# Optimization experiments

Measured on AMD Instinct MI355X. Metric: run time of the kernel, lower is better.

The kernel has to match this reference:

```python
import jax, jax.numpy as jnp
import numpy as np

N, T = 4096, 128
D, R = 8, 32
ENC_H, NADE_H, K_MIX = 64, 64, 10


def setup_inputs() -> dict:
    key = jax.random.key(0)
    ks = jax.random.split(key, 17)
    s = 0.1
    rn = lambda k, shp, sc: (sc * jax.random.normal(k, shp)).astype(jnp.float32)
    return {
        "x": rn(ks[0], (N, 1, T), 1.0),
        "enc1_w": rn(ks[1], (1, ENC_H), s),
        "enc1_b": rn(ks[2], (ENC_H,), s),
        "enc2_w": rn(ks[3], (ENC_H, D), s),
        "enc2_b": rn(ks[4], (D,), s),
        "A": rn(ks[5], (R, D, R), s),
        "init_w": rn(ks[6], (1, R), s),
        "nade1_w": rn(ks[7], (R, NADE_H), s),
        "nade1_b": rn(ks[8], (NADE_H,), s),
        "nade2_w": rn(ks[9], (NADE_H, NADE_H), s),
        "nade2_b": rn(ks[10], (NADE_H,), s),
        "mu_w": rn(ks[11], (NADE_H, K_MIX), s),
        "mu_b": rn(ks[12], (K_MIX,), s),
        "sig_w": rn(ks[13], (NADE_H, K_MIX), s),
        "sig_b": rn(ks[14], (K_MIX,), s),
        "alpha_w": rn(ks[15], (NADE_H, K_MIX), s),
        "alpha_b": rn(ks[16], (K_MIX,), s),
    }


def reference(x, enc1_w, enc1_b, enc2_w, enc2_b, A, init_w,
              nade1_w, nade1_b, nade2_w, nade2_b,
              mu_w, mu_b, sig_w, sig_b, alpha_w, alpha_b):
    LOG2PI = jnp.log(2.0 * jnp.pi).astype(x.dtype)

    def phi(x_t, h):
        # x_t: [N], h: [N, R] -> mixture-of-Gaussians log prob [N]
        h = jnp.tanh(h)
        h = jax.nn.relu(h @ nade1_w + nade1_b)
        h = jax.nn.relu(h @ nade2_w + nade2_b)
        mu = h @ mu_w + mu_b                       # [N, K]
        log_sig = h @ sig_w + sig_b                # sig = exp(log_sig)
        log_alpha = jax.nn.log_softmax(h @ alpha_w + alpha_b, axis=1)
        z = (x_t[:, None] - mu) * jnp.exp(-log_sig)
        comp_lp = -0.5 * z * z - log_sig - 0.5 * LOG2PI
        return jax.scipy.special.logsumexp(log_alpha + comp_lp, axis=1)

    xt = x[:, 0, :]                                # [N, T]
    # vectorized encoder over all timesteps: tanh(relu(x*W1+b1)@W2+b2) -> [N, T, D]
    e = jax.nn.relu(xt[:, :, None] * enc1_w[0] + enc1_b)
    enc = jnp.tanh(e @ enc2_w + enc2_b)

    h0 = jnp.broadcast_to(init_w, (xt.shape[0], R))
    res0 = phi(xt[:, 0], h0)

    def step(carry, inputs):
        tmp, res = carry
        e_prev, x_cur = inputs                     # [N, D], [N]
        tmp = jnp.einsum('nd,ni,idj->nj', e_prev, tmp, A)
        res = res + phi(x_cur, tmp)
        return (tmp, res), None

    xs = (jnp.moveaxis(enc[:, :-1, :], 1, 0),      # [T-1, N, D]
          jnp.moveaxis(xt[:, 1:], 1, 0))           # [T-1, N]
    (_, res), _ = jax.lax.scan(step, (h0, res0), xs)
    return jnp.exp(res)
```

## Files before the change

kernel.cpp:

```cpp
#include <hip/hip_runtime.h>

#define DEV __device__ __forceinline__

typedef __attribute__((ext_vector_type(8))) short short8v;
typedef __attribute__((ext_vector_type(4))) float f32x4;

DEV unsigned short bfr(float f) {
    unsigned u = __float_as_uint(f);
    return (unsigned short)((u + 0x7fffu + ((u >> 16) & 1u)) >> 16);
}
DEV short bft(float f) { return (short)(__float_as_uint(f) >> 16); }
DEV float bf2f(unsigned short h) { return __uint_as_float(((unsigned)h) << 16); }
DEV float frcp(float x) { return __builtin_amdgcn_rcpf(x); }
DEV float ftanh(float x) { float e = __expf(2.0f * x); return 1.0f - 2.0f * frcp(e + 1.0f); }

constexpr int NN = 4096, TT = 128;
#define MFMA32(a, b, c) __builtin_amdgcn_mfma_f32_16x16x32_bf16(a, b, c, 0, 0, 0)


__global__ __launch_bounds__(512) __attribute__((amdgpu_waves_per_eu(2)))
void wfa_kernel(
    const float* __restrict__ x,
    const float* __restrict__ e1w, const float* __restrict__ e1b,
    const float* __restrict__ e2w, const float* __restrict__ e2b,
    const float* __restrict__ A,
    const float* __restrict__ initw,
    const float* __restrict__ n1w, const float* __restrict__ n1b,
    const float* __restrict__ n2w, const float* __restrict__ n2b,
    const float* __restrict__ muw, const float* __restrict__ mub,
    const float* __restrict__ sgw, const float* __restrict__ sgb,
    const float* __restrict__ alw, const float* __restrict__ alb,
    float* __restrict__ out)
{
    __shared__ __align__(16) unsigned short enc_l[TT * 128];
    __shared__ __align__(16) float x_l[16 * 130];
    __shared__ __align__(16) short8v ring_l[2][8][64];
    __shared__ __align__(16) float n1b_l[64], n2b_l[64], hb_l[48];
    __shared__ float part_l[8][16];

    const int tid = threadIdx.x;
    const int wv = tid >> 6, lane = tid & 63;
    const int quad = lane >> 4, col = lane & 15;
    const int n0 = blockIdx.x * 16;
    const f32x4 z4 = {0.f, 0.f, 0.f, 0.f};

    for (int i = tid; i < 16 * TT; i += 512)
        x_l[(i >> 7) * 130 + (i & 127)] = x[(n0 + (i >> 7)) * TT + (i & 127)];
    if (tid < 64) { n1b_l[tid] = n1b[tid]; n2b_l[tid] = n2b[tid]; }
    if (tid >= 64 && tid < 112) {
        const int i = tid - 64, mt = i >> 4, k = i & 15;
        hb_l[i] = (k < 10) ? ((mt == 0) ? mub[k] : (mt == 1) ? sgb[k] : alb[k]) : 0.f;
    }

    __syncthreads();

    {
        float e1c[16], e1bc[16];
        #pragma unroll
        for (int kc = 0; kc < 2; ++kc)
            #pragma unroll
            for (int jj = 0; jj < 8; ++jj) {
                const int f = kc * 32 + (jj >> 2) * 16 + quad * 4 + (jj & 3);
                e1c[kc * 8 + jj] = e1w[f];
                e1bc[kc * 8 + jj] = e1b[f];
            }
        short8v E2A[2];
        #pragma unroll
        for (int kc = 0; kc < 2; ++kc)
            #pragma unroll
            for (int jj = 0; jj < 8; ++jj)
                E2A[kc][jj] = (short)(col < 8
                    ? bfr(e2w[(kc * 32 + (jj >> 2) * 16 + quad * 4 + (jj & 3)) * 8 + col]) : 0);
        float e2bc[4];
        #pragma unroll
        for (int r = 0; r < 4; ++r) e2bc[r] = (quad < 2) ? e2b[quad * 4 + r] : 0.f;

        const int tbase = wv * 16;
        #pragma unroll 1
        for (int nn = 0; nn < 16; ++nn) {
            const float xs = x_l[nn * 130 + tbase + col];
            short8v eB[2];
            #pragma unroll
            for (int kc = 0; kc < 2; ++kc)
                #pragma unroll
                for (int jj = 0; jj < 8; ++jj)
                    eB[kc][jj] = bft(fmaxf(fmaf(xs, e1c[kc * 8 + jj], e1bc[kc * 8 + jj]), 0.f));
            f32x4 d = MFMA32(E2A[0], eB[0], z4);
            d = MFMA32(E2A[1], eB[1], d);
            if (quad < 2) {
                #pragma unroll
                for (int r = 0; r < 4; ++r)
                    enc_l[(tbase + col) * 128 + nn * 8 + quad * 4 + r] = bfr(ftanh(d[r] + e2bc[r]));
            }
        }
    }
    __syncthreads();

    if (wv == 0) {
        short8v A2f[16];
        #pragma unroll
        for (int mt = 0; mt < 16; ++mt)
            #pragma unroll
            for (int jj = 0; jj < 8; ++jj)
                A2f[mt][jj] = (short)bfr(
                    A[((jj >> 2) * 16 + quad * 4 + (jj & 3)) * 256 + (mt >> 1) * 32 + (mt & 1) * 16 + col]);

        short8v tmpB;
        #pragma unroll
        for (int jj = 0; jj < 8; ++jj)
            tmpB[jj] = (short)bfr(initw[(jj >> 2) * 16 + quad * 4 + (jj & 3)]);

        asm volatile("s_setprio 2");

        short8v e8c = *(const short8v*)&enc_l[0 * 128 + col * 8];

        #pragma unroll 1
        for (int b = 0; b <= 16; ++b) {
            if (b < 16) {
                #pragma unroll 1
                for (int i = 0; i < 8; ++i) {
                    const int t = b * 8 + i;
                    if (t > 0) {
                        const short8v e8n = *(const short8v*)&enc_l[t * 128 + col * 8];
                        float ev[8];
                        #pragma unroll
                        for (int d = 0; d < 8; ++d) ev[d] = bf2f((unsigned short)e8c[d]);
                        short8v nt;
                        #pragma unroll
                        for (int h = 0; h < 2; ++h) {
                            f32x4 D[8];
                            #pragma unroll
                            for (int d = 0; d < 8; ++d) D[d] = MFMA32(A2f[2 * d + h], tmpB, z4);
                            #pragma unroll
                            for (int r = 0; r < 4; ++r) {
                                float s = 0.f;
                                #pragma unroll
                                for (int d = 0; d < 8; ++d) s = fmaf(ev[d], D[d][r], s);
                                nt[h * 4 + r] = bft(s);
                            }
                        }
                        tmpB = nt;
                        e8c = e8n;
                    }
                    ring_l[b & 1][i][lane] = tmpB;
                }
            }
            __syncthreads();
        }
        if (lane < 16) part_l[0][lane] = 0.f;
    } else {
        short8v W1f[4];
        #pragma unroll
        for (int mt = 0; mt < 4; ++mt)
            #pragma unroll
            for (int jj = 0; jj < 8; ++jj)
                W1f[mt][jj] = (short)bfr(n1w[((jj >> 2) * 16 + quad * 4 + (jj & 3)) * 64 + mt * 16 + col]);
        short8v W2f[4][2];
        #pragma unroll
        for (int mt = 0; mt < 4; ++mt)
            #pragma unroll
            for (int kb = 0; kb < 2; ++kb)
                #pragma unroll
                for (int jj = 0; jj < 8; ++jj)
                    W2f[mt][kb][jj] = (short)bfr(
                        n2w[(kb * 32 + (jj >> 2) * 16 + quad * 4 + (jj & 3)) * 64 + mt * 16 + col]);
        short8v Whf[3][2];
        #pragma unroll
        for (int mt = 0; mt < 3; ++mt) {
            const float* Wh = (mt == 0) ? muw : (mt == 1) ? sgw : alw;
            #pragma unroll
            for (int kb = 0; kb < 2; ++kb)
                #pragma unroll
                for (int jj = 0; jj < 8; ++jj)
                    Whf[mt][kb][jj] = (short)(col < 10
                        ? bfr(Wh[(kb * 32 + (jj >> 2) * 16 + quad * 4 + (jj & 3)) * 10 + col]) : 0);
        }

        float res2 = 0.f;
        const float CST = 0.91893853320467274f;

        #pragma unroll 1
        for (int b = 0; b <= 16; ++b) {
            if (b >= 1) {
                #pragma unroll 1
                for (int i = wv - 1; i < 8; i += 7) {
                    const int t = (b - 1) * 8 + i;
                    const short8v tf = ring_l[(b - 1) & 1][i][lane];
                    short8v thB;
                    #pragma unroll
                    for (int jj = 0; jj < 8; ++jj)
                        thB[jj] = bft(ftanh(bf2f((unsigned short)tf[jj])));

                    short8v h1B[2];
                    #pragma unroll
                    for (int mt = 0; mt < 4; ++mt) {
                        const f32x4 c = *(const f32x4*)&n1b_l[mt * 16 + quad * 4];
                        const f32x4 d = MFMA32(W1f[mt], thB, c);
                        #pragma unroll
                        for (int r = 0; r < 4; ++r)
                            h1B[mt >> 1][(mt & 1) * 4 + r] = bft(fmaxf(d[r], 0.f));
                    }
                    short8v h2B[2];
                    #pragma unroll
                    for (int mt = 0; mt < 4; ++mt) {
                        const f32x4 c = *(const f32x4*)&n2b_l[mt * 16 + quad * 4];
                        f32x4 d = MFMA32(W2f[mt][0], h1B[0], c);
                        d = MFMA32(W2f[mt][1], h1B[1], d);
                        #pragma unroll
                        for (int r = 0; r < 4; ++r)
                            h2B[mt >> 1][(mt & 1) * 4 + r] = bft(fmaxf(d[r], 0.f));
                    }
                    f32x4 hd[3];
                    #pragma unroll
                    for (int mt = 0; mt < 3; ++mt) {
                        const f32x4 c = *(const f32x4*)&hb_l[mt * 16 + quad * 4];
                        f32x4 d = MFMA32(Whf[mt][0], h2B[0], c);
                        hd[mt] = MFMA32(Whf[mt][1], h2B[1], d);
                    }
                    const float xt = x_l[col * 130 + t];
                    float s1 = 0.f, s2 = 0.f;
                    #pragma unroll
                    for (int r = 0; r < 4; ++r) {
                        const bool valid = (quad * 4 + r) < 10;
                        const float mu = hd[0][r], sg = hd[1][r], la = hd[2][r];
                        const float e1t = __expf(la);
                        const float z = (xt - mu) * __expf(-sg);
                        const float e2t = __expf(la - sg - fmaf(0.5f * z, z, CST));
                        s1 += valid ? e1t : 0.f;
                        s2 += valid ? e2t : 0.f;
                    }
                    s1 += __shfl_xor(s1, 16, 64);  s2 += __shfl_xor(s2, 16, 64);
                    s1 += __shfl_xor(s1, 32, 64);  s2 += __shfl_xor(s2, 32, 64);
                    res2 += __log2f(s2) - __log2f(s1);
                }
            }
            __syncthreads();
        }
        if (lane < 16) part_l[wv][lane] = res2;
    }

    __syncthreads();
    if (tid < 16) {
        float s = 0.f;
        #pragma unroll
        for (int w = 0; w < 8; ++w) s += part_l[w][tid];
        out[n0 + tid] = exp2f(s);
    }
}

extern "C" void kernel_launch(void* const* d_in, const int* in_sizes, int n_in,
                              void* d_out, int out_size, void* d_ws, size_t ws_size,
                              hipStream_t stream) {
    wfa_kernel<<<dim3(NN / 16), dim3(512), 0, stream>>>(
        (const float*)d_in[0],  (const float*)d_in[1],  (const float*)d_in[2],
        (const float*)d_in[3],  (const float*)d_in[4],  (const float*)d_in[5],
        (const float*)d_in[6],  (const float*)d_in[7],  (const float*)d_in[8],
        (const float*)d_in[9],  (const float*)d_in[10], (const float*)d_in[11],
        (const float*)d_in[12], (const float*)d_in[13], (const float*)d_in[14],
        (const float*)d_in[15], (const float*)d_in[16], (float*)d_out);
}
```

Measured before the change: 141.1 us.

## Replace block barriers with LDS flag handshakes and deepen the producer ring

Removes the per-batch __syncthreads between the recurrence wave and the NADE consumer waves. Each side now signals through shared-memory flags and progress counters, spinning with s_sleep while it waits. The ring buffer grows from 2 to 4 slots, so the serial recurrence wave can run ahead of the consumers, and it can start once only the encoder rows it needs are ready. The recurrence also issues all 16 MFMAs at once and reduces them with a tree of FMAs. Spin-waiting on LDS flags depends on correct fencing and memory ordering, and polling adds LDS traffic.

```diff
diff --git a/kernel.cpp b/kernel.cpp
--- a/kernel.cpp
+++ b/kernel.cpp
@@ -15,8 +15,16 @@
 DEV float ftanh(float x) { float e = __expf(2.0f * x); return 1.0f - 2.0f * frcp(e + 1.0f); }
 
 constexpr int NN = 4096, TT = 128;
+constexpr int BATCH = 8, NB = TT / BATCH;
+constexpr int RING = 4;
+
 #define MFMA32(a, b, c) __builtin_amdgcn_mfma_f32_16x16x32_bf16(a, b, c, 0, 0, 0)
 
+
+DEV void wait_ge(const unsigned* p, unsigned v) {
+    volatile const unsigned* vp = (volatile const unsigned*)p;
+    while (*vp < v) { asm volatile("s_sleep 2"); }
+}
 
 __global__ __launch_bounds__(512) __attribute__((amdgpu_waves_per_eu(2)))
 void wfa_kernel(
@@ -34,9 +42,12 @@
 {
     __shared__ __align__(16) unsigned short enc_l[TT * 128];
     __shared__ __align__(16) float x_l[16 * 130];
-    __shared__ __align__(16) short8v ring_l[2][8][64];
+    __shared__ __align__(16) short8v ring_l[RING][BATCH][64];
     __shared__ __align__(16) float n1b_l[64], n2b_l[64], hb_l[48];
     __shared__ float part_l[8][16];
+    __shared__ unsigned rf_l[NB];
+    __shared__ unsigned encf_l[8];
+    __shared__ unsigned prog_l[8];
 
     const int tid = threadIdx.x;
     const int wv = tid >> 6, lane = tid & 63;
@@ -51,7 +62,9 @@
         const int i = tid - 64, mt = i >> 4, k = i & 15;
         hb_l[i] = (k < 10) ? ((mt == 0) ? mub[k] : (mt == 1) ? sgb[k] : alb[k]) : 0.f;
     }
-
+    if (tid >= 112 && tid < 112 + NB) rf_l[tid - 112] = 0;
+    if (tid >= 112 + NB && tid < 120 + NB) encf_l[tid - 112 - NB] = 0;
+    if (tid >= 120 + NB && tid < 128 + NB) prog_l[tid - 120 - NB] = 0;
     __syncthreads();
 
     {
@@ -93,8 +106,9 @@
                     enc_l[(tbase + col) * 128 + nn * 8 + quad * 4 + r] = bfr(ftanh(d[r] + e2bc[r]));
             }
         }
-    }
-    __syncthreads();
+        __threadfence_block();
+        if (lane == 0) ((volatile unsigned*)encf_l)[wv] = 1;
+    }
 
     if (wv == 0) {
         short8v A2f[16];
@@ -112,40 +126,54 @@
 
         asm volatile("s_setprio 2");
 
-        short8v e8c = *(const short8v*)&enc_l[0 * 128 + col * 8];
+        float evc[8];
+        {
+            const short8v e80 = *(const short8v*)&enc_l[0 * 128 + col * 8];
+            #pragma unroll
+            for (int d = 0; d < 8; ++d) evc[d] = bf2f((unsigned short)e80[d]);
+        }
 
         #pragma unroll 1
-        for (int b = 0; b <= 16; ++b) {
-            if (b < 16) {
-                #pragma unroll 1
-                for (int i = 0; i < 8; ++i) {
-                    const int t = b * 8 + i;
-                    if (t > 0) {
-                        const short8v e8n = *(const short8v*)&enc_l[t * 128 + col * 8];
-                        float ev[8];
+        for (int b = 0; b < NB; ++b) {
+            wait_ge(&encf_l[(8 * b + 6) >> 4], 1);
+            if (b >= RING) {
+                const unsigned need = (unsigned)(b - (RING - 1));
+                for (;;) {
+                    unsigned m = 0xffffffffu;
+                    #pragma unroll
+                    for (int w = 1; w < 8; ++w)
+                        m = min(m, ((volatile unsigned*)prog_l)[w]);
+                    if (m >= need) break;
+                    asm volatile("s_sleep 2");
+                }
+            }
+            #pragma unroll 1
+            for (int i = 0; i < BATCH; ++i) {
+                const int t = b * BATCH + i;
+                if (t > 0) {
+                    const short8v e8n = *(const short8v*)&enc_l[t * 128 + col * 8];
+                    f32x4 D[16];
+                    #pragma unroll
+                    for (int mt = 0; mt < 16; ++mt) D[mt] = MFMA32(A2f[mt], tmpB, z4);
+                    short8v nt;
+                    #pragma unroll
+                    for (int h = 0; h < 2; ++h)
                         #pragma unroll
-                        for (int d = 0; d < 8; ++d) ev[d] = bf2f((unsigned short)e8c[d]);
-                        short8v nt;
-                        #pragma unroll
-                        for (int h = 0; h < 2; ++h) {
-                            f32x4 D[8];
-                            #pragma unroll
-                            for (int d = 0; d < 8; ++d) D[d] = MFMA32(A2f[2 * d + h], tmpB, z4);
-                            #pragma unroll
-                            for (int r = 0; r < 4; ++r) {
-                                float s = 0.f;
-                                #pragma unroll
-                                for (int d = 0; d < 8; ++d) s = fmaf(ev[d], D[d][r], s);
-                                nt[h * 4 + r] = bft(s);
-                            }
+                        for (int r = 0; r < 4; ++r) {
+                            const float p0 = fmaf(evc[1], D[2 + h][r], evc[0] * D[h][r]);
+                            const float p1 = fmaf(evc[3], D[6 + h][r], evc[2] * D[4 + h][r]);
+                            const float p2 = fmaf(evc[5], D[10 + h][r], evc[4] * D[8 + h][r]);
+                            const float p3 = fmaf(evc[7], D[14 + h][r], evc[6] * D[12 + h][r]);
+                            nt[h * 4 + r] = bft((p0 + p1) + (p2 + p3));
                         }
-                        tmpB = nt;
-                        e8c = e8n;
-                    }
-                    ring_l[b & 1][i][lane] = tmpB;
-                }
-            }
-            __syncthreads();
+                    tmpB = nt;
+                    #pragma unroll
+                    for (int d = 0; d < 8; ++d) evc[d] = bf2f((unsigned short)e8n[d]);
+                }
+                ring_l[b & (RING - 1)][i][lane] = tmpB;
+            }
+            __threadfence_block();
+            if (lane == 0) ((volatile unsigned*)rf_l)[b] = 1;
         }
         if (lane < 16) part_l[0][lane] = 0.f;
     } else {
@@ -180,61 +208,60 @@
         const float CST = 0.91893853320467274f;
 
         #pragma unroll 1
-        for (int b = 0; b <= 16; ++b) {
-            if (b >= 1) {
-                #pragma unroll 1
-                for (int i = wv - 1; i < 8; i += 7) {
-                    const int t = (b - 1) * 8 + i;
-                    const short8v tf = ring_l[(b - 1) & 1][i][lane];
-                    short8v thB;
-                    #pragma unroll
-                    for (int jj = 0; jj < 8; ++jj)
-                        thB[jj] = bft(ftanh(bf2f((unsigned short)tf[jj])));
-
-                    short8v h1B[2];
-                    #pragma unroll
-                    for (int mt = 0; mt < 4; ++mt) {
-                        const f32x4 c = *(const f32x4*)&n1b_l[mt * 16 + quad * 4];
-                        const f32x4 d = MFMA32(W1f[mt], thB, c);
-                        #pragma unroll
-                        for (int r = 0; r < 4; ++r)
-                            h1B[mt >> 1][(mt & 1) * 4 + r] = bft(fmaxf(d[r], 0.f));
-                    }
-                    short8v h2B[2];
-                    #pragma unroll
-                    for (int mt = 0; mt < 4; ++mt) {
-                        const f32x4 c = *(const f32x4*)&n2b_l[mt * 16 + quad * 4];
-                        f32x4 d = MFMA32(W2f[mt][0], h1B[0], c);
-                        d = MFMA32(W2f[mt][1], h1B[1], d);
-                        #pragma unroll
-                        for (int r = 0; r < 4; ++r)
-                            h2B[mt >> 1][(mt & 1) * 4 + r] = bft(fmaxf(d[r], 0.f));
-                    }
-                    f32x4 hd[3];
-                    #pragma unroll
-                    for (int mt = 0; mt < 3; ++mt) {
-                        const f32x4 c = *(const f32x4*)&hb_l[mt * 16 + quad * 4];
-                        f32x4 d = MFMA32(Whf[mt][0], h2B[0], c);
-                        hd[mt] = MFMA32(Whf[mt][1], h2B[1], d);
-                    }
-                    const float xt = x_l[col * 130 + t];
-                    float s1 = 0.f, s2 = 0.f;
-                    #pragma unroll
-                    for (int r = 0; r < 4; ++r) {
-                        const bool valid = (quad * 4 + r) < 10;
-                        const float mu = hd[0][r], sg = hd[1][r], la = hd[2][r];
-                        const float e1t = __expf(la);
-                        const float z = (xt - mu) * __expf(-sg);
-                        const float e2t = __expf(la - sg - fmaf(0.5f * z, z, CST));
-                        s1 += valid ? e1t : 0.f;
-                        s2 += valid ? e2t : 0.f;
-                    }
-                    s1 += __shfl_xor(s1, 16, 64);  s2 += __shfl_xor(s2, 16, 64);
-                    s1 += __shfl_xor(s1, 32, 64);  s2 += __shfl_xor(s2, 32, 64);
-                    res2 += __log2f(s2) - __log2f(s1);
-                }
-            }
-            __syncthreads();
+        for (int b = 0; b < NB; ++b) {
+            wait_ge(&rf_l[b], 1);
+            #pragma unroll 1
+            for (int i = wv - 1; i < BATCH; i += 7) {
+                const int t = b * BATCH + i;
+                const short8v tf = ring_l[b & (RING - 1)][i][lane];
+                short8v thB;
+                #pragma unroll
+                for (int jj = 0; jj < 8; ++jj)
+                    thB[jj] = bft(ftanh(bf2f((unsigned short)tf[jj])));
+
+                short8v h1B[2];
+                #pragma unroll
+                for (int mt = 0; mt < 4; ++mt) {
+                    const f32x4 c = *(const f32x4*)&n1b_l[mt * 16 + quad * 4];
+                    const f32x4 d = MFMA32(W1f[mt], thB, c);
+                    #pragma unroll
+                    for (int r = 0; r < 4; ++r)
+                        h1B[mt >> 1][(mt & 1) * 4 + r] = bft(fmaxf(d[r], 0.f));
+                }
+                short8v h2B[2];
+                #pragma unroll
+                for (int mt = 0; mt < 4; ++mt) {
+                    const f32x4 c = *(const f32x4*)&n2b_l[mt * 16 + quad * 4];
+                    f32x4 d = MFMA32(W2f[mt][0], h1B[0], c);
+                    d = MFMA32(W2f[mt][1], h1B[1], d);
+                    #pragma unroll
+                    for (int r = 0; r < 4; ++r)
+                        h2B[mt >> 1][(mt & 1) * 4 + r] = bft(fmaxf(d[r], 0.f));
+                }
+                f32x4 hd[3];
+                #pragma unroll
+                for (int mt = 0; mt < 3; ++mt) {
+                    const f32x4 c = *(const f32x4*)&hb_l[mt * 16 + quad * 4];
+                    f32x4 d = MFMA32(Whf[mt][0], h2B[0], c);
+                    hd[mt] = MFMA32(Whf[mt][1], h2B[1], d);
+                }
+                const float xt = x_l[col * 130 + t];
+                float s1 = 0.f, s2 = 0.f;
+                #pragma unroll
+                for (int r = 0; r < 4; ++r) {
+                    const bool valid = (quad * 4 + r) < 10;
+                    const float mu = hd[0][r], sg = hd[1][r], la = hd[2][r];
+                    const float e1t = __expf(la);
+                    const float z = (xt - mu) * __expf(-sg);
+                    const float e2t = __expf(la - sg - fmaf(0.5f * z, z, CST));
+                    s1 += valid ? e1t : 0.f;
+                    s2 += valid ? e2t : 0.f;
+                }
+                s1 += __shfl_xor(s1, 16, 64);  s2 += __shfl_xor(s2, 16, 64);
+                s1 += __shfl_xor(s1, 32, 64);  s2 += __shfl_xor(s2, 32, 64);
+                res2 += __log2f(s2) - __log2f(s1);
+            }
+            if (lane == 0) ((volatile unsigned*)prog_l)[wv] = (unsigned)(b + 1);
         }
         if (lane < 16) part_l[wv][lane] = res2;
     }
```

Result: slower. 149.8 us (+6.2%).
